# Optimization experiments

Measured on AMD Instinct MI355X. Metric: run time of the kernel, lower is better.

The kernel has to match this reference:

```python
import jax, jax.numpy as jnp
import numpy as np
import math

D_EMB = 1024
N_HEADS = 16
D_HEAD = D_EMB // N_HEADS
D_FF = 4 * D_EMB
BATCH = 2
SEQ = 2048
EPS = 1e-6


def setup_inputs() -> dict:
    key = jax.random.key(0)
    ks = jax.random.split(key, 12)
    s = 0.02
    return {
        "x": jax.random.normal(ks[0], (BATCH, SEQ, D_EMB), jnp.float32),
        "wq": jax.random.normal(ks[1], (D_EMB, D_EMB), jnp.float32) * s,
        "wk": jax.random.normal(ks[2], (D_EMB, D_EMB), jnp.float32) * s,
        "wv": jax.random.normal(ks[3], (D_EMB, D_EMB), jnp.float32) * s,
        "wo": jax.random.normal(ks[4], (D_EMB, D_EMB), jnp.float32) * s,
        "bo": jnp.zeros((D_EMB,), jnp.float32),
        "w1": jax.random.normal(ks[5], (D_FF, D_EMB), jnp.float32) * s,
        "b1": jnp.zeros((D_FF,), jnp.float32),
        "w2": jax.random.normal(ks[6], (D_EMB, D_FF), jnp.float32) * s,
        "b2": jnp.zeros((D_EMB,), jnp.float32),
        "ln1_s": jnp.ones((D_EMB,), jnp.float32),
        "ln1_b": jnp.zeros((D_EMB,), jnp.float32),
        "ln2_s": jnp.ones((D_EMB,), jnp.float32),
        "ln2_b": jnp.zeros((D_EMB,), jnp.float32),
    }


def _layernorm(x, scale, shift):
    mean = jnp.mean(x, axis=-1, keepdims=True)
    var = jnp.mean(jnp.square(x - mean), axis=-1, keepdims=True)  # unbiased=False
    return scale * (x - mean) / jnp.sqrt(var + EPS) + shift


def _gelu_tanh(x):
    c = math.sqrt(2.0 / math.pi)
    return 0.5 * x * (1.0 + jnp.tanh(c * (x + 0.044715 * x * x * x)))


def _attention(x, wq, wk, wv, wo, bo):
    B, S, _ = x.shape
    q = (x @ wq.T).reshape(B, S, N_HEADS, D_HEAD).transpose(0, 2, 1, 3)
    k = (x @ wk.T).reshape(B, S, N_HEADS, D_HEAD).transpose(0, 2, 1, 3)
    v = (x @ wv.T).reshape(B, S, N_HEADS, D_HEAD).transpose(0, 2, 1, 3)
    scores = jnp.einsum("bhqd,bhkd->bhqk", q, k)
    causal = jnp.triu(jnp.ones((S, S), bool), k=1)
    scores = jnp.where(causal, -jnp.inf, scores)
    weights = jax.nn.softmax(scores / math.sqrt(D_HEAD), axis=-1)
    ctx = jnp.einsum("bhqk,bhkd->bhqd", weights, v)
    ctx = ctx.transpose(0, 2, 1, 3).reshape(B, S, D_EMB)
    return ctx @ wo.T + bo


def reference(x, wq, wk, wv, wo, bo, w1, b1, w2, b2, ln1_s, ln1_b, ln2_s, ln2_b):
    # pre-norm attention block (dropout in eval mode = identity)
    h = x + _attention(_layernorm(x, ln1_s, ln1_b), wq, wk, wv, wo, bo)
    # pre-norm MLP with tanh-approx GeLU
    y = _layernorm(h, ln2_s, ln2_b)
    y = _gelu_tanh(y @ w1.T + b1) @ w2.T + b2
    return h + y
```

## Files before the change

kernel.cpp:

```cpp
#include <hip/hip_runtime.h>
#include <math.h>

typedef unsigned short u16;
typedef __attribute__((ext_vector_type(8))) __bf16 bf16x8v;
typedef __attribute__((ext_vector_type(8))) unsigned short ushort8v;
typedef __attribute__((ext_vector_type(4))) unsigned short ushort4v;
typedef __attribute__((ext_vector_type(4))) float f32x4v;

#define D_EMBD 1024
#define NHEADS 16
#define DHEAD  64
#define DFF    4096
#define BATCHN 2
#define SEQL   2048
#define TOK    (BATCHN*SEQL)

#define EPI_BF16_GELU    2
#define EPI_BF16_QKV     3
#define EPI_BF16_PART    5

__device__ __forceinline__ float bf2f(u16 s) {
  return __builtin_bit_cast(float, (unsigned)s << 16);
}
__device__ __forceinline__ u16 f2bf(float f) {
  unsigned u = __builtin_bit_cast(unsigned, f);
  unsigned r = u + 0x7fffu + ((u >> 16) & 1u);
  return (u16)(r >> 16);
}
__device__ __forceinline__ u16 f2bf_trunc(float f) {
  return (u16)(__builtin_bit_cast(unsigned, f) >> 16);
}

#define GLOAD16(gp, lp)                                                        \
  __builtin_amdgcn_global_load_lds(                                            \
      (__attribute__((address_space(1))) void*)(void*)(gp),                    \
      (__attribute__((address_space(3))) void*)(void*)(lp), 16, 0, 0)

__global__ __launch_bounds__(256) void cvt_all_kernel(const float* __restrict__ wq,
                                                      const float* __restrict__ wk,
                                                      const float* __restrict__ wv,
                                                      const float* __restrict__ wo,
                                                      const float* __restrict__ w1,
                                                      const float* __restrict__ w2,
                                                      u16* __restrict__ wcat,
                                                      u16* __restrict__ wob,
                                                      u16* __restrict__ w1b,
                                                      u16* __restrict__ w2b) {
  int bid = blockIdx.x;
  const float* src;
  u16* dst;
  int loc;
  if (bid < 4096) {
    int seg = bid >> 10;
    loc = (bid & 1023) * 256 + threadIdx.x;
    src = (seg == 0) ? wq : (seg == 1) ? wk : (seg == 2) ? wv : wo;
    dst = (seg == 0) ? wcat : (seg == 1) ? wcat + 1048576
                            : (seg == 2) ? wcat + 2097152 : wob;
  } else if (bid < 8192) {
    loc = (bid - 4096) * 256 + threadIdx.x;
    src = w1; dst = w1b;
  } else {
    loc = (bid - 8192) * 256 + threadIdx.x;
    src = w2; dst = w2b;
  }
  float4 v = ((const float4*)src)[loc];
  ushort4 o;
  o.x = f2bf(v.x); o.y = f2bf(v.y); o.z = f2bf(v.z); o.w = f2bf(v.w);
  ((ushort4*)dst)[loc] = o;
}

__global__ __launch_bounds__(256) void ln_kernel(const float* __restrict__ x,
                                                 const float* __restrict__ sc,
                                                 const float* __restrict__ sh,
                                                 u16* __restrict__ out) {
  int row = blockIdx.x, tid = threadIdx.x;
  const float4* xr = (const float4*)(x + (size_t)row * D_EMBD);
  float4 v = xr[tid];
  float s  = (v.x + v.y) + (v.z + v.w);
  float s2 = (v.x * v.x + v.y * v.y) + (v.z * v.z + v.w * v.w);
#pragma unroll
  for (int off = 32; off; off >>= 1) {
    s  += __shfl_xor(s, off, 64);
    s2 += __shfl_xor(s2, off, 64);
  }
  __shared__ float rs[4], rs2[4];
  int wave = tid >> 6, lane = tid & 63;
  if (lane == 0) { rs[wave] = s; rs2[wave] = s2; }
  __syncthreads();
  s  = (rs[0] + rs[1]) + (rs[2] + rs[3]);
  s2 = (rs2[0] + rs2[1]) + (rs2[2] + rs2[3]);
  float mean = s * (1.f / 1024.f);
  float var  = s2 * (1.f / 1024.f) - mean * mean;
  float rstd = rsqrtf(var + 1e-6f);
  float4 scv = ((const float4*)sc)[tid];
  float4 shv = ((const float4*)sh)[tid];
  ushort4 o;
  o.x = f2bf((v.x - mean) * rstd * scv.x + shv.x);
  o.y = f2bf((v.y - mean) * rstd * scv.y + shv.y);
  o.z = f2bf((v.z - mean) * rstd * scv.z + shv.z);
  o.w = f2bf((v.w - mean) * rstd * scv.w + shv.w);
  ((ushort4*)(out + (size_t)row * D_EMBD))[tid] = o;
}

__global__ __launch_bounds__(256) void ln2f_kernel(const u16* __restrict__ parts,
                                                   const float* __restrict__ x,
                                                   const float* __restrict__ bo,
                                                   const float* __restrict__ sc,
                                                   const float* __restrict__ sh,
                                                   float* __restrict__ hbuf,
                                                   u16* __restrict__ ybuf) {
  int row = blockIdx.x, tid = threadIdx.x;
  size_t base4 = (size_t)row * 256 + tid;
  float4 v = ((const float4*)x)[base4];
  float4 bv = ((const float4*)bo)[tid];
  v.x += bv.x; v.y += bv.y; v.z += bv.z; v.w += bv.w;
#pragma unroll
  for (int p = 0; p < 4; ++p) {
    ushort4 u = ((const ushort4*)parts)[(size_t)p * 1048576 + base4];
    v.x += bf2f(u.x); v.y += bf2f(u.y); v.z += bf2f(u.z); v.w += bf2f(u.w);
  }
  ((float4*)hbuf)[base4] = v;
  float s  = (v.x + v.y) + (v.z + v.w);
  float s2 = (v.x * v.x + v.y * v.y) + (v.z * v.z + v.w * v.w);
#pragma unroll
  for (int off = 32; off; off >>= 1) {
    s  += __shfl_xor(s, off, 64);
    s2 += __shfl_xor(s2, off, 64);
  }
  __shared__ float rs[4], rs2[4];
  int wave = tid >> 6, lane = tid & 63;
  if (lane == 0) { rs[wave] = s; rs2[wave] = s2; }
  __syncthreads();
  s  = (rs[0] + rs[1]) + (rs[2] + rs[3]);
  s2 = (rs2[0] + rs2[1]) + (rs2[2] + rs2[3]);
  float mean = s * (1.f / 1024.f);
  float var  = s2 * (1.f / 1024.f) - mean * mean;
  float rstd = rsqrtf(var + 1e-6f);
  float4 scv = ((const float4*)sc)[tid];
  float4 shv = ((const float4*)sh)[tid];
  ushort4 o;
  o.x = f2bf((v.x - mean) * rstd * scv.x + shv.x);
  o.y = f2bf((v.y - mean) * rstd * scv.y + shv.y);
  o.z = f2bf((v.z - mean) * rstd * scv.z + shv.z);
  o.w = f2bf((v.w - mean) * rstd * scv.w + shv.w);
  ((ushort4*)ybuf)[base4] = o;
}

__global__ __launch_bounds__(256) void reduce_w2_kernel(const u16* __restrict__ parts,
                                                        const float* __restrict__ resid,
                                                        const float* __restrict__ bias,
                                                        float* __restrict__ out) {
  int i = blockIdx.x * 256 + threadIdx.x;
  float4 r = ((const float4*)resid)[i];
  float4 bi = ((const float4*)bias)[i & 255];
  float s0 = 0, s1 = 0, s2 = 0, s3 = 0;
#pragma unroll
  for (int p = 0; p < 4; ++p) {
    ushort4 u = ((const ushort4*)parts)[(size_t)p * 1048576 + i];
    s0 += bf2f(u.x); s1 += bf2f(u.y); s2 += bf2f(u.z); s3 += bf2f(u.w);
  }
  float4 o = {s0 + r.x + bi.x, s1 + r.y + bi.y, s2 + r.z + bi.z, s3 + r.w + bi.w};
  ((float4*)out)[i] = o;
}

template <int MH, int NH, bool READA, class FS, class FG>
__device__ __forceinline__ void gphase(const u16* sm, int cur, int wm, int wn,
                                       int lr, int quad,
                                       f32x4v (&acc)[8][4], bf16x8v (&av)[4][2],
                                       FS&& st, FG&& gate) {
  const int sx = lr & 7;
  bf16x8v bv[2][2];
  if constexpr (READA) {
#pragma unroll
    for (int j2 = 0; j2 < 4; ++j2) {
      int g = 2 * (MH * 4 + j2) + wm;
      int row = g * 16 + lr;
#pragma unroll
      for (int kk = 0; kk < 2; ++kk) {
        int slot = (kk * 4 + quad) ^ sx;
        av[j2][kk] = *(const bf16x8v*)(sm + cur * 32768 + row * 64 + slot * 8);
      }
    }
  }
#pragma unroll
  for (int i2 = 0; i2 < 2; ++i2) {
    int h = wn + 4 * (NH * 2 + i2);
    int row = h * 16 + lr;
#pragma unroll
    for (int kk = 0; kk < 2; ++kk) {
      int slot = (kk * 4 + quad) ^ sx;
      bv[i2][kk] = *(const bf16x8v*)(sm + cur * 32768 + 16384 + row * 64 + slot * 8);
    }
  }
  st();
  gate();
  __builtin_amdgcn_s_barrier();
  asm volatile("s_waitcnt lgkmcnt(0)" ::: "memory");
  __builtin_amdgcn_sched_barrier(0);
  __builtin_amdgcn_s_setprio(1);
#pragma unroll
  for (int j2 = 0; j2 < 4; ++j2)
#pragma unroll
    for (int i2 = 0; i2 < 2; ++i2)
#pragma unroll
      for (int kk = 0; kk < 2; ++kk)
        acc[MH * 4 + j2][NH * 2 + i2] = __builtin_amdgcn_mfma_f32_16x16x32_bf16(
            av[j2][kk], bv[i2][kk], acc[MH * 4 + j2][NH * 2 + i2], 0, 0, 0);
  __builtin_amdgcn_s_setprio(0);
  __builtin_amdgcn_sched_barrier(0);
  __builtin_amdgcn_s_barrier();
}

template <int EPI>
__global__ __launch_bounds__(512, 2) void gemm256(const u16* __restrict__ A,
                                                  const u16* __restrict__ W,
                                                  u16* __restrict__ Cb,
                                                  const float* __restrict__ bias,
                                                  int M, int N, int K) {
  __shared__ __align__(16) u16 sm[65536];
  const int tid = threadIdx.x;
  const int wave = tid >> 6, lane = tid & 63;
  const int lr = lane & 15, quad = lane >> 4;
  const int wm = wave >> 2, wn = wave & 3;
  const int m0 = blockIdx.y * 256, n0 = blockIdx.x * 256;
  const int KC = K / gridDim.z;
  const int kbeg = blockIdx.z * KC;
  const int NT = KC >> 6;
  const size_t poff = (size_t)blockIdx.z * ((size_t)M * N);

  const int r8 = lane >> 3;
  const int sslot = (lane & 7) ^ r8;
  const int rb0 = wave * 2;

  auto stA = [&](int bb, int h, int tk) {
#pragma unroll
    for (int s = 0; s < 2; ++s) {
      const u16* gp = A + (size_t)(m0 + h * 128 + (rb0 + s) * 8 + r8) * K +
                      (kbeg + tk * 64 + sslot * 8);
      GLOAD16(gp, (char*)sm + bb * 65536 + h * 16384 + (rb0 + s) * 1024);
    }
  };
  auto stB = [&](int bb, int h, int tk) {
#pragma unroll
    for (int s = 0; s < 2; ++s) {
      const u16* gp = W + (size_t)(n0 + h * 128 + (rb0 + s) * 8 + r8) * K +
                      (kbeg + tk * 64 + sslot * 8);
      GLOAD16(gp, (char*)sm + bb * 65536 + 32768 + h * 16384 + (rb0 + s) * 1024);
    }
  };

  f32x4v acc[8][4];
#pragma unroll
  for (int j = 0; j < 8; ++j)
#pragma unroll
    for (int i = 0; i < 4; ++i) {
      f32x4v z = {0.f, 0.f, 0.f, 0.f};
      acc[j][i] = z;
    }
  bf16x8v av[4][2];

  stA(0, 0, 0); stB(0, 0, 0); stA(0, 1, 0); stB(0, 1, 0);
  stA(1, 0, 1); stB(1, 1, 1);
  asm volatile("s_waitcnt vmcnt(4)" ::: "memory");
  __builtin_amdgcn_s_barrier();

  for (int t = 0; t < NT; ++t) {
    const int cur = t & 1, nb = cur ^ 1;
    const bool p1 = (t + 1 < NT), p2 = (t + 2 < NT);
    gphase<0, 0, true>(sm, cur, wm, wn, lr, quad, acc, av,
        [&] { if (p1) stB(nb, 0, t + 1); }, [&] {});
    gphase<0, 1, false>(sm, cur, wm, wn, lr, quad, acc, av,
        [&] { if (p1) stA(nb, 1, t + 1); }, [&] {});
    gphase<1, 1, true>(sm, cur, wm, wn, lr, quad, acc, av,
        [&] { if (p2) stA(cur, 0, t + 2); }, [&] {});
    gphase<1, 0, false>(sm, cur, wm, wn, lr, quad, acc, av,
        [&] { if (p2) stB(cur, 1, t + 2); },
        [&] {
          if (p2) { asm volatile("s_waitcnt vmcnt(4)" ::: "memory"); }
          else    { asm volatile("s_waitcnt vmcnt(0)" ::: "memory"); }
        });
  }

  const bool qsc = (EPI == EPI_BF16_QKV) && (n0 < 1024);
#pragma unroll
  for (int j = 0; j < 8; ++j) {
    int gr = m0 + (2 * j + wm) * 16 + quad * 4;
#pragma unroll
    for (int i = 0; i < 4; ++i) {
      int gc = n0 + (wn + 4 * i) * 16 + lr;
      float bi = 0.f;
      if constexpr (EPI == EPI_BF16_GELU) bi = bias[gc];
#pragma unroll
      for (int r = 0; r < 4; ++r) {
        size_t idx = (size_t)(gr + r) * N + gc;
        float v = acc[j][i][r];
        if constexpr (EPI == EPI_BF16_PART) {
          Cb[poff + idx] = f2bf(v);
        } else if constexpr (EPI == EPI_BF16_QKV) {
          Cb[idx] = f2bf(qsc ? v * 0.125f : v);
        } else {
          v += bi;
          float z = 0.7978845608028654f * (v + 0.044715f * v * v * v);
          float tt = 2.f / (1.f + __expf(-2.f * z)) - 1.f;
          Cb[idx] = f2bf(0.5f * v * (1.f + tt));
        }
      }
    }
  }
}

#define VTS 72
__device__ __forceinline__ void stage_k(const u16* Kbase, int ks, u16* kfbuf,
                                        int wave, int lr, int quad) {
#pragma unroll
  for (int p = 0; p < 2; ++p) {
    int q = wave * 2 + p;
    int key = ((q >> 1) << 4) + lr;
    int c8 = ((q & 1) << 2) + quad;
    GLOAD16(Kbase + (size_t)(ks + key) * 3072 + c8 * 8, (char*)kfbuf + q * 1024);
  }
}
__device__ __forceinline__ void load_v(const u16* Vbase, int ks, int vkey0, int vc8,
                                       ushort8v& va, ushort8v& vb) {
  va = *(const ushort8v*)(Vbase + (size_t)(ks + vkey0) * 3072 + vc8 * 8);
  vb = *(const ushort8v*)(Vbase + (size_t)(ks + vkey0 + 1) * 3072 + vc8 * 8);
}
__device__ __forceinline__ void write_vt(u16* vt, int vc8, int vcol,
                                         ushort8v va, ushort8v vb) {
#pragma unroll
  for (int j = 0; j < 8; ++j) {
    unsigned pk = (unsigned)va[j] | ((unsigned)vb[j] << 16);
    *(unsigned*)(vt + (size_t)(vc8 * 8 + j) * VTS + vcol) = pk;
  }
}

__global__ __launch_bounds__(256) void attn_kernel(const u16* __restrict__ qkv,
                                                   u16* __restrict__ ctx) {
  __shared__ u16 Kf[2][4096];
  __shared__ u16 Vt[2][64 * VTS];
  int tid = threadIdx.x;
  int wave = tid >> 6, lane = tid & 63;
  int lr = lane & 15, quad = lane >> 4;
  int id = blockIdx.x;
  int bh = id & 31;
  int t = 31 - (id >> 5);
  int b = bh >> 4, h = bh & 15;
  int q0 = t * 64;
  const u16* qkvb = qkv + (size_t)(b * SEQL) * 3072;
  int qrow = q0 + wave * 16 + lr;
  const u16* Qp = qkvb + (size_t)qrow * 3072 + h * 64 + quad * 8;
  bf16x8v qf0 = *(const bf16x8v*)(Qp);
  bf16x8v qf1 = *(const bf16x8v*)(Qp + 32);
  const u16* Kbase = qkvb + 1024 + h * 64;
  const u16* Vbase = qkvb + 2048 + h * 64;
  int vkey0 = (tid >> 3) * 2, vc8 = tid & 7;
  int vcol = vkey0 ^ (vc8 << 2);

  float m = -INFINITY, l = 0.f;
  f32x4v accO[4];
#pragma unroll
  for (int r = 0; r < 4; r++) {
    f32x4v z = {0.f, 0.f, 0.f, 0.f};
    accO[r] = z;
  }

  int nkt = t + 1;
  {
    stage_k(Kbase, 0, Kf[0], wave, lr, quad);
    ushort8v va, vb;
    load_v(Vbase, 0, vkey0, vc8, va, vb);
    write_vt(Vt[0], vc8, vcol, va, vb);
  }
  __syncthreads();

  for (int kt = 0; kt < nkt; ++kt) {
    int cur = kt & 1, nxt = cur ^ 1;
    ushort8v va, vb;
    bool pre = (kt + 1 < nkt);
    if (pre) {
      stage_k(Kbase, (kt + 1) * 64, Kf[nxt], wave, lr, quad);
      load_v(Vbase, (kt + 1) * 64, vkey0, vc8, va, vb);
    }
    const bf16x8v* Kc = (const bf16x8v*)Kf[cur];
    const u16* Vc = Vt[cur];
    f32x4v accS[4];
#pragma unroll
    for (int jb = 0; jb < 4; jb++) {
      f32x4v z = {0.f, 0.f, 0.f, 0.f};
      accS[jb] = z;
    }
#pragma unroll
    for (int jb = 0; jb < 4; jb++) {
      accS[jb] = __builtin_amdgcn_mfma_f32_16x16x32_bf16(Kc[((jb * 2 + 0) << 6) + lane], qf0, accS[jb], 0, 0, 0);
      accS[jb] = __builtin_amdgcn_mfma_f32_16x16x32_bf16(Kc[((jb * 2 + 1) << 6) + lane], qf1, accS[jb], 0, 0, 0);
    }
    if (kt == t) {
#pragma unroll
      for (int jb = 0; jb < 4; jb++)
#pragma unroll
        for (int r = 0; r < 4; r++)
          if (jb * 16 + quad * 4 + r > wave * 16 + lr) accS[jb][r] = -INFINITY;
    }
    float smax = accS[0][0];
#pragma unroll
    for (int jb = 0; jb < 4; jb++)
#pragma unroll
      for (int r = 0; r < 4; r++) smax = fmaxf(smax, accS[jb][r]);
    smax = fmaxf(smax, __shfl_xor(smax, 16, 64));
    smax = fmaxf(smax, __shfl_xor(smax, 32, 64));
    float mn = fmaxf(m, smax);
    float alpha = __expf(m - mn);
    m = mn;
    float ps = 0.f;
#pragma unroll
    for (int jb = 0; jb < 4; jb++)
#pragma unroll
      for (int r = 0; r < 4; r++) {
        accS[jb][r] = __expf(accS[jb][r] - mn);
        ps += accS[jb][r];
      }
    ps += __shfl_xor(ps, 16, 64);
    ps += __shfl_xor(ps, 32, 64);
    l = l * alpha + ps;
    float ar[4];
#pragma unroll
    for (int r = 0; r < 4; r++) ar[r] = __shfl(alpha, quad * 4 + r, 16);
#pragma unroll
    for (int nb = 0; nb < 4; nb++)
#pragma unroll
      for (int r = 0; r < 4; r++) accO[nb][r] *= ar[r];
#pragma unroll
    for (int kk = 0; kk < 2; ++kk) {
      ushort8v pp;
#pragma unroll
      for (int j = 0; j < 4; ++j) {
        pp[j]     = f2bf_trunc(accS[2 * kk][j]);
        pp[j + 4] = f2bf_trunc(accS[2 * kk + 1][j]);
      }
      bf16x8v pav = __builtin_bit_cast(bf16x8v, pp);
#pragma unroll
      for (int nb = 0; nb < 4; nb++) {
        int dim = nb * 16 + lr;
        int f = (nb * 2 + (lr >> 3)) & 7;
        int col1 = (kk * 32 + quad * 4) ^ (f << 2);
        ushort4v v0 = *(const ushort4v*)(Vc + dim * VTS + col1);
        ushort4v v1 = *(const ushort4v*)(Vc + dim * VTS + (col1 ^ 16));
        ushort8v vv;
#pragma unroll
        for (int j = 0; j < 4; ++j) { vv[j] = v0[j]; vv[j + 4] = v1[j]; }
        accO[nb] = __builtin_amdgcn_mfma_f32_16x16x32_bf16(pav, __builtin_bit_cast(bf16x8v, vv), accO[nb], 0, 0, 0);
      }
    }
    if (pre) write_vt(Vt[nxt], vc8, vcol, va, vb);
    __syncthreads();
  }
  float linv = 1.f / l;
  float rr[4];
#pragma unroll
  for (int r = 0; r < 4; r++) rr[r] = __shfl(linv, quad * 4 + r, 16);
#pragma unroll
  for (int nb = 0; nb < 4; nb++)
#pragma unroll
    for (int r = 0; r < 4; r++) {
      int rowg = q0 + wave * 16 + quad * 4 + r;
      ctx[(size_t)(b * SEQL + rowg) * D_EMBD + h * 64 + nb * 16 + lr] =
          f2bf(accO[nb][r] * rr[r]);
    }
}

extern "C" void kernel_launch(void* const* d_in, const int* in_sizes, int n_in,
                              void* d_out, int out_size, void* d_ws, size_t ws_size,
                              hipStream_t stream) {
  const float* x    = (const float*)d_in[0];
  const float* wq   = (const float*)d_in[1];
  const float* wk   = (const float*)d_in[2];
  const float* wv   = (const float*)d_in[3];
  const float* wo   = (const float*)d_in[4];
  const float* bo   = (const float*)d_in[5];
  const float* w1   = (const float*)d_in[6];
  const float* b1   = (const float*)d_in[7];
  const float* w2   = (const float*)d_in[8];
  const float* b2   = (const float*)d_in[9];
  const float* ln1s = (const float*)d_in[10];
  const float* ln1b = (const float*)d_in[11];
  const float* ln2s = (const float*)d_in[12];
  const float* ln2b = (const float*)d_in[13];
  float* out = (float*)d_out;

  char* base = (char*)d_ws;
  size_t off = 0;
  auto alloc = [&](size_t bytes) {
    char* r = base + off;
    off += (bytes + 255) & ~(size_t)255;
    return r;
  };
  u16*   wcat = (u16*)alloc((size_t)3072 * 1024 * 2);
  u16*   wob  = (u16*)alloc((size_t)1024 * 1024 * 2);
  u16*   w1b  = (u16*)alloc((size_t)4096 * 1024 * 2);
  u16*   w2b  = (u16*)alloc((size_t)1024 * 4096 * 2);
  u16*   xn   = (u16*)alloc((size_t)TOK * 1024 * 2);
  u16*   qkv  = (u16*)alloc((size_t)TOK * 3072 * 2);
  u16*   ctx  = (u16*)alloc((size_t)TOK * 1024 * 2);
  float* hbuf = (float*)alloc((size_t)TOK * 1024 * 4);
  u16*   ybuf = (u16*)alloc((size_t)TOK * 1024 * 2);
  u16*   gbuf = (u16*)alloc((size_t)TOK * 4096 * 2);
  u16* woP = (u16*)xn;
  u16* w2P = (u16*)xn;

  cvt_all_kernel<<<12288, 256, 0, stream>>>(wq, wk, wv, wo, w1, w2,
                                            wcat, wob, w1b, w2b);
  ln_kernel<<<TOK, 256, 0, stream>>>(x, ln1s, ln1b, xn);
  gemm256<EPI_BF16_QKV><<<dim3(12, 16), 512, 0, stream>>>(
      xn, wcat, qkv, nullptr, TOK, 3072, 1024);
  attn_kernel<<<1024, 256, 0, stream>>>(qkv, ctx);
  gemm256<EPI_BF16_PART><<<dim3(4, 16, 4), 512, 0, stream>>>(
      ctx, wob, woP, nullptr, TOK, 1024, 1024);
  ln2f_kernel<<<TOK, 256, 0, stream>>>(woP, x, bo, ln2s, ln2b, hbuf, ybuf);
  gemm256<EPI_BF16_GELU><<<dim3(16, 16), 512, 0, stream>>>(
      ybuf, w1b, gbuf, b1, TOK, 4096, 1024);
  gemm256<EPI_BF16_PART><<<dim3(4, 16, 4), 512, 0, stream>>>(
      gbuf, w2b, w2P, nullptr, TOK, 1024, 4096);
  reduce_w2_kernel<<<4096, 256, 0, stream>>>(w2P, hbuf, b2, out);
}
```

Measured before the change: 336.7 us.

## Use 128-query tiles with 8 waves in attention to share K/V staging

The attention kernel now handles 128 query rows per block with 512 threads (8 waves) instead of 64 rows with 4 waves, which halves the grid. Each staged 64-key K/V tile is reused by twice as many query rows, roughly halving global reads of K/V and the LDS transpose work per query. Only the first 256 threads stage V. The first four waves skip the last key tile, which lies entirely above their causal diagonal. The trade-offs are fewer blocks for load balancing across CUs and idle waves on the final tile.

After: 339.4 us. About the same (+0.8%).

```diff
diff --git a/kernel.cpp b/kernel.cpp
--- a/kernel.cpp
+++ b/kernel.cpp
@@ -310,15 +310,11 @@
 }
 
 #define VTS 72
-__device__ __forceinline__ void stage_k(const u16* Kbase, int ks, u16* kfbuf,
-                                        int wave, int lr, int quad) {
-#pragma unroll
-  for (int p = 0; p < 2; ++p) {
-    int q = wave * 2 + p;
-    int key = ((q >> 1) << 4) + lr;
-    int c8 = ((q & 1) << 2) + quad;
-    GLOAD16(Kbase + (size_t)(ks + key) * 3072 + c8 * 8, (char*)kfbuf + q * 1024);
-  }
+__device__ __forceinline__ void stage_k8(const u16* Kbase, int ks, u16* kfbuf,
+                                         int wave, int lr, int quad) {
+  int key = ((wave >> 1) << 4) + lr;
+  int c8 = ((wave & 1) << 2) + quad;
+  GLOAD16(Kbase + (size_t)(ks + key) * 3072 + c8 * 8, (char*)kfbuf + wave * 1024);
 }
 __device__ __forceinline__ void load_v(const u16* Vbase, int ks, int vkey0, int vc8,
                                        ushort8v& va, ushort8v& vb) {
@@ -334,7 +330,7 @@
   }
 }
 
-__global__ __launch_bounds__(256) void attn_kernel(const u16* __restrict__ qkv,
+__global__ __launch_bounds__(512) void attn_kernel(const u16* __restrict__ qkv,
                                                    u16* __restrict__ ctx) {
   __shared__ u16 Kf[2][4096];
   __shared__ u16 Vt[2][64 * VTS];
@@ -343,9 +339,9 @@
   int lr = lane & 15, quad = lane >> 4;
   int id = blockIdx.x;
   int bh = id & 31;
-  int t = 31 - (id >> 5);
+  int t = 15 - (id >> 5);
   int b = bh >> 4, h = bh & 15;
-  int q0 = t * 64;
+  int q0 = t * 128;
   const u16* qkvb = qkv + (size_t)(b * SEQL) * 3072;
   int qrow = q0 + wave * 16 + lr;
   const u16* Qp = qkvb + (size_t)qrow * 3072 + h * 64 + quad * 8;
@@ -353,7 +349,8 @@
   bf16x8v qf1 = *(const bf16x8v*)(Qp + 32);
   const u16* Kbase = qkvb + 1024 + h * 64;
   const u16* Vbase = qkvb + 2048 + h * 64;
-  int vkey0 = (tid >> 3) * 2, vc8 = tid & 7;
+  const bool vstager = (tid < 256);
+  int vkey0 = ((tid & 255) >> 3) * 2, vc8 = tid & 7;
   int vcol = vkey0 ^ (vc8 << 2);
 
   float m = -INFINITY, l = 0.f;
@@ -364,12 +361,14 @@
     accO[r] = z;
   }
 
-  int nkt = t + 1;
+  int nkt = 2 * t + 2;
   {
-    stage_k(Kbase, 0, Kf[0], wave, lr, quad);
-    ushort8v va, vb;
-    load_v(Vbase, 0, vkey0, vc8, va, vb);
-    write_vt(Vt[0], vc8, vcol, va, vb);
+    stage_k8(Kbase, 0, Kf[0], wave, lr, quad);
+    if (vstager) {
+      ushort8v va, vb;
+      load_v(Vbase, 0, vkey0, vc8, va, vb);
+      write_vt(Vt[0], vc8, vcol, va, vb);
+    }
   }
   __syncthreads();
 
@@ -378,80 +377,84 @@
     ushort8v va, vb;
     bool pre = (kt + 1 < nkt);
     if (pre) {
-      stage_k(Kbase, (kt + 1) * 64, Kf[nxt], wave, lr, quad);
-      load_v(Vbase, (kt + 1) * 64, vkey0, vc8, va, vb);
-    }
-    const bf16x8v* Kc = (const bf16x8v*)Kf[cur];
-    const u16* Vc = Vt[cur];
-    f32x4v accS[4];
-#pragma unroll
-    for (int jb = 0; jb < 4; jb++) {
-      f32x4v z = {0.f, 0.f, 0.f, 0.f};
-      accS[jb] = z;
-    }
-#pragma unroll
-    for (int jb = 0; jb < 4; jb++) {
-      accS[jb] = __builtin_amdgcn_mfma_f32_16x16x32_bf16(Kc[((jb * 2 + 0) << 6) + lane], qf0, accS[jb], 0, 0, 0);
-      accS[jb] = __builtin_amdgcn_mfma_f32_16x16x32_bf16(Kc[((jb * 2 + 1) << 6) + lane], qf1, accS[jb], 0, 0, 0);
-    }
-    if (kt == t) {
+      stage_k8(Kbase, (kt + 1) * 64, Kf[nxt], wave, lr, quad);
+      if (vstager) load_v(Vbase, (kt + 1) * 64, vkey0, vc8, va, vb);
+    }
+    bool active = !(kt == 2 * t + 1 && wave < 4);
+    if (active) {
+      const bf16x8v* Kc = (const bf16x8v*)Kf[cur];
+      const u16* Vc = Vt[cur];
+      f32x4v accS[4];
+#pragma unroll
+      for (int jb = 0; jb < 4; jb++) {
+        f32x4v z = {0.f, 0.f, 0.f, 0.f};
+        accS[jb] = z;
+      }
+#pragma unroll
+      for (int jb = 0; jb < 4; jb++) {
+        accS[jb] = __builtin_amdgcn_mfma_f32_16x16x32_bf16(Kc[((jb * 2 + 0) << 6) + lane], qf0, accS[jb], 0, 0, 0);
+        accS[jb] = __builtin_amdgcn_mfma_f32_16x16x32_bf16(Kc[((jb * 2 + 1) << 6) + lane], qf1, accS[jb], 0, 0, 0);
+      }
+      if (kt >= 2 * t) {
+        int kb = (kt - 2 * t) << 6;
+#pragma unroll
+        for (int jb = 0; jb < 4; jb++)
+#pragma unroll
+          for (int r = 0; r < 4; r++)
+            if (kb + jb * 16 + quad * 4 + r > wave * 16 + lr) accS[jb][r] = -INFINITY;
+      }
+      float smax = accS[0][0];
 #pragma unroll
       for (int jb = 0; jb < 4; jb++)
 #pragma unroll
-        for (int r = 0; r < 4; r++)
-          if (jb * 16 + quad * 4 + r > wave * 16 + lr) accS[jb][r] = -INFINITY;
-    }
-    float smax = accS[0][0];
-#pragma unroll
-    for (int jb = 0; jb < 4; jb++)
-#pragma unroll
-      for (int r = 0; r < 4; r++) smax = fmaxf(smax, accS[jb][r]);
-    smax = fmaxf(smax, __shfl_xor(smax, 16, 64));
-    smax = fmaxf(smax, __shfl_xor(smax, 32, 64));
-    float mn = fmaxf(m, smax);
-    float alpha = __expf(m - mn);
-    m = mn;
-    float ps = 0.f;
-#pragma unroll
-    for (int jb = 0; jb < 4; jb++)
-#pragma unroll
-      for (int r = 0; r < 4; r++) {
-        accS[jb][r] = __expf(accS[jb][r] - mn);
-        ps += accS[jb][r];
+        for (int r = 0; r < 4; r++) smax = fmaxf(smax, accS[jb][r]);
+      smax = fmaxf(smax, __shfl_xor(smax, 16, 64));
+      smax = fmaxf(smax, __shfl_xor(smax, 32, 64));
+      float mn = fmaxf(m, smax);
+      float alpha = __expf(m - mn);
+      m = mn;
+      float ps = 0.f;
+#pragma unroll
+      for (int jb = 0; jb < 4; jb++)
+#pragma unroll
+        for (int r = 0; r < 4; r++) {
+          accS[jb][r] = __expf(accS[jb][r] - mn);
+          ps += accS[jb][r];
+        }
+      ps += __shfl_xor(ps, 16, 64);
+      ps += __shfl_xor(ps, 32, 64);
+      l = l * alpha + ps;
+      float ar[4];
+#pragma unroll
+      for (int r = 0; r < 4; r++) ar[r] = __shfl(alpha, quad * 4 + r, 16);
+#pragma unroll
+      for (int nb = 0; nb < 4; nb++)
+#pragma unroll
+        for (int r = 0; r < 4; r++) accO[nb][r] *= ar[r];
+#pragma unroll
+      for (int kk = 0; kk < 2; ++kk) {
+        ushort8v pp;
+#pragma unroll
+        for (int j = 0; j < 4; ++j) {
+          pp[j]     = f2bf_trunc(accS[2 * kk][j]);
+          pp[j + 4] = f2bf_trunc(accS[2 * kk + 1][j]);
+        }
+        bf16x8v pav = __builtin_bit_cast(bf16x8v, pp);
+#pragma unroll
+        for (int nb = 0; nb < 4; nb++) {
+          int dim = nb * 16 + lr;
+          int f = (nb * 2 + (lr >> 3)) & 7;
+          int col1 = (kk * 32 + quad * 4) ^ (f << 2);
+          ushort4v v0 = *(const ushort4v*)(Vc + dim * VTS + col1);
+          ushort4v v1 = *(const ushort4v*)(Vc + dim * VTS + (col1 ^ 16));
+          ushort8v vv;
+#pragma unroll
+          for (int j = 0; j < 4; ++j) { vv[j] = v0[j]; vv[j + 4] = v1[j]; }
+          accO[nb] = __builtin_amdgcn_mfma_f32_16x16x32_bf16(pav, __builtin_bit_cast(bf16x8v, vv), accO[nb], 0, 0, 0);
+        }
       }
-    ps += __shfl_xor(ps, 16, 64);
-    ps += __shfl_xor(ps, 32, 64);
-    l = l * alpha + ps;
-    float ar[4];
-#pragma unroll
-    for (int r = 0; r < 4; r++) ar[r] = __shfl(alpha, quad * 4 + r, 16);
-#pragma unroll
-    for (int nb = 0; nb < 4; nb++)
-#pragma unroll
-      for (int r = 0; r < 4; r++) accO[nb][r] *= ar[r];
-#pragma unroll
-    for (int kk = 0; kk < 2; ++kk) {
-      ushort8v pp;
-#pragma unroll
-      for (int j = 0; j < 4; ++j) {
-        pp[j]     = f2bf_trunc(accS[2 * kk][j]);
-        pp[j + 4] = f2bf_trunc(accS[2 * kk + 1][j]);
-      }
-      bf16x8v pav = __builtin_bit_cast(bf16x8v, pp);
-#pragma unroll
-      for (int nb = 0; nb < 4; nb++) {
-        int dim = nb * 16 + lr;
-        int f = (nb * 2 + (lr >> 3)) & 7;
-        int col1 = (kk * 32 + quad * 4) ^ (f << 2);
-        ushort4v v0 = *(const ushort4v*)(Vc + dim * VTS + col1);
-        ushort4v v1 = *(const ushort4v*)(Vc + dim * VTS + (col1 ^ 16));
-        ushort8v vv;
-#pragma unroll
-        for (int j = 0; j < 4; ++j) { vv[j] = v0[j]; vv[j + 4] = v1[j]; }
-        accO[nb] = __builtin_amdgcn_mfma_f32_16x16x32_bf16(pav, __builtin_bit_cast(bf16x8v, vv), accO[nb], 0, 0, 0);
-      }
-    }
-    if (pre) write_vt(Vt[nxt], vc8, vcol, va, vb);
+    }
+    if (pre && vstager) write_vt(Vt[nxt], vc8, vcol, va, vb);
     __syncthreads();
   }
   float linv = 1.f / l;
@@ -512,7 +515,7 @@
   ln_kernel<<<TOK, 256, 0, stream>>>(x, ln1s, ln1b, xn);
   gemm256<EPI_BF16_QKV><<<dim3(12, 16), 512, 0, stream>>>(
       xn, wcat, qkv, nullptr, TOK, 3072, 1024);
-  attn_kernel<<<1024, 256, 0, stream>>>(qkv, ctx);
+  attn_kernel<<<512, 512, 0, stream>>>(qkv, ctx);
   gemm256<EPI_BF16_PART><<<dim3(4, 16, 4), 512, 0, stream>>>(
       ctx, wob, woP, nullptr, TOK, 1024, 1024);
   ln2f_kernel<<<TOK, 256, 0, stream>>>(woP, x, bo, ln2s, ln2b, hbuf, ybuf);
```
